# Kernel tuning notes

Measured on AMD Instinct MI355X. Metric: run time of the kernel, lower is better.

Reference implementation:

```python
import jax, jax.numpy as jnp
import numpy as np

UNITS = 512
M = 8
INPUT_DIM = 512
BATCH = 2048


def setup_inputs() -> dict:
    key = jax.random.key(0)
    ks = jax.random.split(key, 9)
    D, U = INPUT_DIM, UNITS
    fused_dim = D + U
    def glorot(k, shape):
        lim = np.sqrt(6.0 / (shape[0] + shape[1])).astype(np.float32)
        return jax.random.uniform(k, shape, jnp.float32, -lim, lim)
    return {
        "inputs": jax.random.normal(ks[0], (BATCH, D), jnp.float32),
        "elapsed": jax.random.uniform(ks[1], (BATCH, 1), jnp.float32),
        "state": jax.random.normal(ks[2], (BATCH, U * M), jnp.float32),
        "W_r": glorot(ks[3], (fused_dim, U * M)),
        "b_r": jnp.zeros((U * M,), jnp.float32),
        "W_d": glorot(ks[4], (fused_dim, U)),
        "b_d": jnp.zeros((U,), jnp.float32),
        "W_u": glorot(ks[5], (fused_dim, U * M)),
        "b_u": jnp.zeros((U * M,), jnp.float32),
    }


def reference(inputs, elapsed, state, W_r, b_r, W_d, b_d, W_u, b_u):
    B = inputs.shape[0]
    # tau_i = 10**(i/2)  =>  ln_tau_i = i * 0.5 * ln(10)
    ln_tau_table = 0.5 * jnp.log(jnp.float32(10.0)) * jnp.arange(M, dtype=jnp.float32)  # [M]
    tau_table = jnp.exp(ln_tau_table)  # [M]

    h_hat = state.reshape(B, UNITS, M)            # [B, U, M]
    h = h_hat.sum(axis=2)                          # [B, U]
    fused = jnp.concatenate([inputs, h], axis=-1)  # [B, D+U]

    # retrieval gate: softmax over M buckets of -(ln_tau_r - table)^2
    ln_tau_r = (fused @ W_r + b_r).reshape(B, UNITS, M)
    rki = jax.nn.softmax(-jnp.square(ln_tau_r - ln_tau_table), axis=2)
    q_input = jnp.sum(rki * h_hat, axis=2)         # [B, U]

    # detect (candidate) with tanh
    reset_value = jnp.concatenate([inputs, q_input], axis=1)
    qk = jnp.tanh(reset_value @ W_d + b_d)[:, :, None]  # [B, U, 1]

    # update gate
    ln_tau_s = (fused @ W_u + b_u).reshape(B, UNITS, M)
    ski = jax.nn.softmax(-jnp.square(ln_tau_s - ln_tau_table), axis=2)

    # exponential decay per bucket: elapsed [B,1] / tau [M] -> [B, M]
    exp_term = jnp.exp(-elapsed / tau_table)[:, None, :]  # [B, 1, M]
    h_hat_next = ((1.0 - ski) * h_hat + ski * qk) * exp_term  # [B, U, M]

    h_next = h_hat_next.sum(axis=2)                # [B, U]
    return h_next, h_hat_next.reshape(B, UNITS * M)
```

## Files before the change

kernel.cpp:

```cpp
#include <hip/hip_runtime.h>
#include <hip/hip_fp16.h>
#include <cmath>

#define B_SZ 2048
#define D_IN 512
#define U_N  512
#define FD   1024
#define NRU  4096
#define NRU2 8192

typedef _Float16 f16x8 __attribute__((ext_vector_type(8)));
typedef float    f32x4 __attribute__((ext_vector_type(4)));

typedef const __attribute__((address_space(1))) void glb_cv;
typedef __attribute__((address_space(3))) void lds_v;

#define TAB_INIT {0.0f, 1.15129254649702f, 2.30258509299405f, \
                  3.45387763949107f, 4.60517018598809f, 5.75646273248511f, \
                  6.90775527898214f, 8.05904782547916f}

__global__ __launch_bounds__(256) void prep_kernel(
    const float* __restrict__ inputs, const float* __restrict__ state,
    __half* __restrict__ fused, __half* __restrict__ reset)
{
    const int b = blockIdx.x;
    const int t = threadIdx.x;

    const float2 iv = *(const float2*)(inputs + (size_t)b * D_IN + t * 2);
    __half2 hv;
    hv.x = __float2half(iv.x);
    hv.y = __float2half(iv.y);
    *(__half2*)(fused + (size_t)b * FD + t * 2) = hv;
    *(__half2*)(reset + (size_t)b * FD + t * 2) = hv;

    const float4* sp = (const float4*)(state + (size_t)b * NRU + t * 16);
    float4 x0 = sp[0], x1 = sp[1], x2 = sp[2], x3 = sp[3];
    float s0 = (x0.x + x0.y) + (x0.z + x0.w) + (x1.x + x1.y) + (x1.z + x1.w);
    float s1 = (x2.x + x2.y) + (x2.z + x2.w) + (x3.x + x3.y) + (x3.z + x3.w);
    __half2 h2;
    h2.x = __float2half(s0);
    h2.y = __float2half(s1);
    *(__half2*)(fused + (size_t)b * FD + D_IN + t * 2) = h2;
}

__global__ __launch_bounds__(256) void convT3_kernel(
    const float* __restrict__ W_r, const float* __restrict__ W_u,
    const float* __restrict__ W_d, __half* __restrict__ WruT,
    __half* __restrict__ WdT)
{
    __shared__ float tile[32][33];
    const int bx = blockIdx.x;
    const float* W;
    __half* Wt;
    int N, nt;
    if (bx < 128)      { W = W_r; Wt = WruT;                        N = NRU; nt = bx * 32; }
    else if (bx < 256) { W = W_u; Wt = WruT + (size_t)NRU * FD;     N = NRU; nt = (bx - 128) * 32; }
    else               { W = W_d; Wt = WdT;                         N = U_N; nt = (bx - 256) * 32; }

    const int kt = blockIdx.y * 32;
    const int t  = threadIdx.x;
    const int c  = t & 31;
    const int r4 = t >> 5;

#pragma unroll
    for (int i = 0; i < 4; i++) {
        int r = r4 + i * 8;
        tile[r][c] = W[(size_t)(kt + r) * N + nt + c];
    }
    __syncthreads();
#pragma unroll
    for (int i = 0; i < 4; i++) {
        int rr = r4 + i * 8;
        Wt[(size_t)(nt + rr) * FD + kt + c] = __float2half(tile[c][rr]);
    }
}

template <int BM, int ACT, int EPI>
__global__ __launch_bounds__(256) void gemm_k(
    const __half* __restrict__ A, const __half* __restrict__ Bt,
    const float* __restrict__ biasA, const float* __restrict__ biasB, int nsplit,
    float* __restrict__ C, int Ncols,
    const float* __restrict__ state, __half* __restrict__ resetw,
    __half* __restrict__ skibuf, int K)
{
    extern __shared__ __align__(16) char smem[];
    __half* sA = (__half*)smem;
    __half* sB = (__half*)(smem + BM * 64);

    const int t    = threadIdx.x;
    const int m0   = blockIdx.y * BM;
    const int n0   = blockIdx.x << 7;
    const int lane = t & 63;
    const int w    = t >> 6;
    const int m16  = lane & 15;
    const int quad = lane >> 4;
    constexpr int MI = BM / 32;
    constexpr int IA = BM / 64;
    const int wm = (w & 1) * (BM / 2);
    const int wn = (w >> 1) << 6;

    f32x4 acc[MI][4];
#pragma unroll
    for (int i = 0; i < MI; i++)
#pragma unroll
        for (int j = 0; j < 4; j++)
#pragma unroll
            for (int r = 0; r < 4; r++) acc[i][j][r] = 0.f;

    const __half* gAp[IA];
    const __half* lAp[IA];
#pragma unroll
    for (int i = 0; i < IA; i++) {
        const int off = w * (BM * 16) + i * 1024 + lane * 16;
        const int row = off >> 6;
        const int kc  = (off & 63) >> 1;
        gAp[i] = A + (size_t)(m0 + row) * K + kc;
        lAp[i] = sA + ((w * (BM * 16) + i * 1024) >> 1);
    }
    const __half* gBp[2];
    const __half* lBp[2];
#pragma unroll
    for (int i = 0; i < 2; i++) {
        const int off = w * 2048 + i * 1024 + lane * 16;
        const int row = off >> 6;
        const int kc  = (off & 63) >> 1;
        gBp[i] = Bt + (size_t)(n0 + row) * K + kc;
        lBp[i] = sB + ((w * 2048 + i * 1024) >> 1);
    }

    for (int kt = 0; kt < K; kt += 32) {
        __syncthreads();
#pragma unroll
        for (int i = 0; i < IA; i++)
            __builtin_amdgcn_global_load_lds((glb_cv*)(gAp[i] + kt), (lds_v*)lAp[i], 16, 0, 0);
#pragma unroll
        for (int i = 0; i < 2; i++)
            __builtin_amdgcn_global_load_lds((glb_cv*)(gBp[i] + kt), (lds_v*)lBp[i], 16, 0, 0);
        __syncthreads();

        f16x8 af[MI], bf[4];
#pragma unroll
        for (int mi = 0; mi < MI; mi++)
            af[mi] = *(const f16x8*)(sA + (wm + mi * 16 + m16) * 32 + quad * 8);
#pragma unroll
        for (int ni = 0; ni < 4; ni++)
            bf[ni] = *(const f16x8*)(sB + (wn + ni * 16 + m16) * 32 + quad * 8);
#pragma unroll
        for (int mi = 0; mi < MI; mi++)
#pragma unroll
            for (int ni = 0; ni < 4; ni++)
                acc[mi][ni] = __builtin_amdgcn_mfma_f32_16x16x32_f16(
                    af[mi], bf[ni], acc[mi][ni], 0, 0, 0);
    }

    if constexpr (EPI == 0) {
        const float* bp  = (n0 < nsplit) ? biasA : biasB;
        const int    cb0 = (n0 < nsplit) ? n0 : n0 - nsplit;
#pragma unroll
        for (int mi = 0; mi < MI; mi++) {
#pragma unroll
            for (int ni = 0; ni < 4; ni++) {
                const int ctile = wn + ni * 16 + m16;
                const float bv = bp[cb0 + ctile];
                const int col = n0 + ctile;
#pragma unroll
                for (int r = 0; r < 4; r++) {
                    const int row = m0 + wm + mi * 16 + quad * 4 + r;
                    float v = acc[mi][ni][r] + bv;
                    if (ACT == 1) v = tanhf(v);
                    C[(size_t)row * Ncols + col] = v;
                }
            }
        }
    } else {
        __syncthreads();
        float* ebuf = (float*)smem + w * (64 * 17);
        const bool is_r = (n0 < nsplit);
        const float* bp = is_r ? biasA : biasB;
        const int cb = (is_r ? n0 : n0 - nsplit) + wn;
        const float TAB[8] = TAB_INIT;

        for (int ni = 0; ni < 4; ni++) {
            const float bv = bp[cb + ni * 16 + m16];
#pragma unroll
            for (int mi = 0; mi < 4; mi++)
#pragma unroll
                for (int r = 0; r < 4; r++)
                    ebuf[(mi * 16 + quad * 4 + r) * 17 + m16] = acc[mi][ni][r] + bv;
            __syncthreads();

            const int b = m0 + wm + lane;
#pragma unroll
            for (int j = 0; j < 2; j++) {
                const float* rowp = ebuf + lane * 17 + j * 8;
                float s[8], e[8];
                float mx = -1e30f;
#pragma unroll
                for (int i = 0; i < 8; i++) {
                    float d = rowp[i] - TAB[i];
                    s[i] = -d * d;
                    mx = fmaxf(mx, s[i]);
                }
                float sum = 0.f;
#pragma unroll
                for (int i = 0; i < 8; i++) {
                    e[i] = __expf(s[i] - mx);
                    sum += e[i];
                }
                const int c0 = cb + ni * 16 + j * 8;
                if (is_r) {
                    const float4* hh = (const float4*)(state + (size_t)b * NRU + c0);
                    float4 h0 = hh[0], h1 = hh[1];
                    float hv[8] = {h0.x, h0.y, h0.z, h0.w, h1.x, h1.y, h1.z, h1.w};
                    float qn = 0.f;
#pragma unroll
                    for (int i = 0; i < 8; i++) qn += e[i] * hv[i];
                    const float q = qn / sum;
                    resetw[(size_t)b * FD + D_IN + (c0 >> 3)] = __float2half(q);
                } else {
                    const float inv = 1.0f / sum;
                    __half2 o[4];
#pragma unroll
                    for (int i = 0; i < 4; i++) {
                        o[i].x = __float2half(e[2 * i] * inv);
                        o[i].y = __float2half(e[2 * i + 1] * inv);
                    }
                    *(uint4*)(skibuf + (size_t)b * NRU + c0) = *(uint4*)o;
                }
            }
            __syncthreads();
        }
    }
}

__global__ __launch_bounds__(256) void final_kernel(
    const __half* __restrict__ skibuf, const float* __restrict__ state,
    const float* __restrict__ qk, const float* __restrict__ elapsed,
    float* __restrict__ out0, float* __restrict__ out1)
{
    const int idx = blockIdx.x * 256 + threadIdx.x;
    const int b = idx >> 9;
    const int u = idx & 511;

    const float INV_TAU[8] = {1.0f, 0.316227766016838f, 0.1f, 0.0316227766016838f,
                              0.01f, 0.00316227766016838f, 0.001f, 0.000316227766016838f};

    const uint4 sr = *(const uint4*)(skibuf + (size_t)b * NRU + u * 8);
    const __half2* sh = (const __half2*)&sr;
    float sk[8];
#pragma unroll
    for (int i = 0; i < 4; i++) {
        sk[2 * i]     = __half2float(sh[i].x);
        sk[2 * i + 1] = __half2float(sh[i].y);
    }

    const float4* hh = (const float4*)(state + ((size_t)b * NRU + u * 8));
    float4 h0 = hh[0], h1 = hh[1];
    float h[8] = {h0.x, h0.y, h0.z, h0.w, h1.x, h1.y, h1.z, h1.w};

    const float q  = qk[(size_t)b * U_N + u];
    const float el = elapsed[b];

    float hn[8];
    float acc = 0.f;
#pragma unroll
    for (int i = 0; i < 8; i++) {
        const float et = __expf(-el * INV_TAU[i]);
        hn[i] = ((1.0f - sk[i]) * h[i] + sk[i] * q) * et;
        acc += hn[i];
    }

    float4* o = (float4*)(out1 + ((size_t)b * NRU + u * 8));
    o[0] = make_float4(hn[0], hn[1], hn[2], hn[3]);
    o[1] = make_float4(hn[4], hn[5], hn[6], hn[7]);
    out0[(size_t)b * U_N + u] = acc;
}

extern "C" void kernel_launch(void* const* d_in, const int* in_sizes, int n_in,
                              void* d_out, int out_size, void* d_ws, size_t ws_size,
                              hipStream_t stream)
{
    (void)in_sizes; (void)n_in; (void)out_size; (void)ws_size;

    const float* inputs  = (const float*)d_in[0];
    const float* elapsed = (const float*)d_in[1];
    const float* state   = (const float*)d_in[2];
    const float* W_r     = (const float*)d_in[3];
    const float* b_r     = (const float*)d_in[4];
    const float* W_d     = (const float*)d_in[5];
    const float* b_d     = (const float*)d_in[6];
    const float* W_u     = (const float*)d_in[7];
    const float* b_u     = (const float*)d_in[8];
    float* out = (float*)d_out;

    char* ws = (char*)d_ws;
    __half* fused  = (__half*)(ws);
    __half* reset  = (__half*)(ws + ((size_t)4  << 20));
    __half* WruT   = (__half*)(ws + ((size_t)8  << 20));
    __half* WdT    = (__half*)(ws + ((size_t)24 << 20));
    __half* skibuf = (__half*)(ws + ((size_t)25 << 20));
    float*  qk     = (float*) (ws + ((size_t)41 << 20));

    prep_kernel<<<B_SZ, 256, 0, stream>>>(inputs, state, fused, reset);
    convT3_kernel<<<dim3(272, FD / 32), 256, 0, stream>>>(W_r, W_u, W_d, WruT, WdT);

    gemm_k<128, 0, 1><<<dim3(NRU2 / 128, B_SZ / 128), 256, 17408, stream>>>(
        fused, WruT, b_r, b_u, NRU, nullptr, 0, state, reset, skibuf, FD);

    gemm_k<64, 1, 0><<<dim3(U_N / 128, B_SZ / 64), 256, 12288, stream>>>(
        reset, WdT, b_d, b_d, 1 << 30, qk, U_N, nullptr, nullptr, nullptr, FD);

    final_kernel<<<(B_SZ * U_N) / 256, 256, 0, stream>>>(skibuf, state, qk, elapsed, out,
                                                         out + (size_t)B_SZ * U_N);
}
```

Baseline: 231.2 us.

## Fuse final state update into detect GEMM epilogue and coalesce softmax epilogue

Result: faster. 225.8 us (-2.3%).

```diff
diff --git a/kernel.cpp b/kernel.cpp
--- a/kernel.cpp
+++ b/kernel.cpp
@@ -53,9 +53,9 @@
     const float* W;
     __half* Wt;
     int N, nt;
-    if (bx < 128)      { W = W_r; Wt = WruT;                        N = NRU; nt = bx * 32; }
-    else if (bx < 256) { W = W_u; Wt = WruT + (size_t)NRU * FD;     N = NRU; nt = (bx - 128) * 32; }
-    else               { W = W_d; Wt = WdT;                         N = U_N; nt = (bx - 256) * 32; }
+    if (bx < 128)      { W = W_r; Wt = WruT;                    N = NRU; nt = bx * 32; }
+    else if (bx < 256) { W = W_u; Wt = WruT + (size_t)NRU * FD; N = NRU; nt = (bx - 128) * 32; }
+    else               { W = W_d; Wt = WdT;                     N = U_N; nt = (bx - 256) * 32; }
 
     const int kt = blockIdx.y * 32;
     const int t  = threadIdx.x;
@@ -75,13 +75,13 @@
     }
 }
 
-template <int BM, int ACT, int EPI>
+template <int BM, int EPI>
 __global__ __launch_bounds__(256) void gemm_k(
     const __half* __restrict__ A, const __half* __restrict__ Bt,
     const float* __restrict__ biasA, const float* __restrict__ biasB, int nsplit,
-    float* __restrict__ C, int Ncols,
     const float* __restrict__ state, __half* __restrict__ resetw,
-    __half* __restrict__ skibuf, int K)
+    __half* __restrict__ skibuf, const float* __restrict__ elapsed,
+    float* __restrict__ out0, float* __restrict__ out1, int K)
 {
     extern __shared__ __align__(16) char smem[];
     __half* sA = (__half*)smem;
@@ -98,6 +98,7 @@
     constexpr int IA = BM / 64;
     const int wm = (w & 1) * (BM / 2);
     const int wn = (w >> 1) << 6;
+    const int strip = w >> 1;
 
     f32x4 acc[MI][4];
 #pragma unroll
@@ -153,70 +154,61 @@
                     af[mi], bf[ni], acc[mi][ni], 0, 0, 0);
     }
 
-    if constexpr (EPI == 0) {
-        const float* bp  = (n0 < nsplit) ? biasA : biasB;
-        const int    cb0 = (n0 < nsplit) ? n0 : n0 - nsplit;
-#pragma unroll
-        for (int mi = 0; mi < MI; mi++) {
-#pragma unroll
-            for (int ni = 0; ni < 4; ni++) {
-                const int ctile = wn + ni * 16 + m16;
-                const float bv = bp[cb0 + ctile];
-                const int col = n0 + ctile;
-#pragma unroll
-                for (int r = 0; r < 4; r++) {
-                    const int row = m0 + wm + mi * 16 + quad * 4 + r;
-                    float v = acc[mi][ni][r] + bv;
-                    if (ACT == 1) v = tanhf(v);
-                    C[(size_t)row * Ncols + col] = v;
-                }
-            }
-        }
-    } else {
+    if constexpr (EPI == 1) {
         __syncthreads();
-        float* ebuf = (float*)smem + w * (64 * 17);
+        float*  ebuf = (float*)smem;
+        __half* qbuf = (__half*)(smem + 128 * 36 * 4);
         const bool is_r = (n0 < nsplit);
         const float* bp = is_r ? biasA : biasB;
-        const int cb = (is_r ? n0 : n0 - nsplit) + wn;
+        const int n0r = is_r ? n0 : n0 - nsplit;
         const float TAB[8] = TAB_INIT;
+        const int ug  = t & 3;
+        const int s   = ug >> 1;
+        const int g   = ug & 1;
+        const int bl0 = t >> 2;
 
         for (int ni = 0; ni < 4; ni++) {
-            const float bv = bp[cb + ni * 16 + m16];
+            const float bv = bp[n0r + strip * 64 + ni * 16 + m16];
 #pragma unroll
             for (int mi = 0; mi < 4; mi++)
 #pragma unroll
                 for (int r = 0; r < 4; r++)
-                    ebuf[(mi * 16 + quad * 4 + r) * 17 + m16] = acc[mi][ni][r] + bv;
+                    ebuf[(wm + mi * 16 + quad * 4 + r) * 36 + strip * 16 + m16] =
+                        acc[mi][ni][r] + bv;
             __syncthreads();
 
-            const int b = m0 + wm + lane;
-#pragma unroll
-            for (int j = 0; j < 2; j++) {
-                const float* rowp = ebuf + lane * 17 + j * 8;
-                float s[8], e[8];
+#pragma unroll
+            for (int p = 0; p < 2; p++) {
+                const int b_loc = bl0 + p * 64;
+                const int b = m0 + b_loc;
+                const float* rowp = ebuf + b_loc * 36 + ug * 8;
+                float v[8];
+                *(float4*)&v[0] = *(const float4*)rowp;
+                *(float4*)&v[4] = *(const float4*)(rowp + 4);
+
+                float sc[8], e[8];
                 float mx = -1e30f;
 #pragma unroll
                 for (int i = 0; i < 8; i++) {
-                    float d = rowp[i] - TAB[i];
-                    s[i] = -d * d;
-                    mx = fmaxf(mx, s[i]);
+                    float d = v[i] - TAB[i];
+                    sc[i] = -d * d;
+                    mx = fmaxf(mx, sc[i]);
                 }
                 float sum = 0.f;
 #pragma unroll
                 for (int i = 0; i < 8; i++) {
-                    e[i] = __expf(s[i] - mx);
+                    e[i] = __expf(sc[i] - mx);
                     sum += e[i];
                 }
-                const int c0 = cb + ni * 16 + j * 8;
+                const int col = n0r + s * 64 + ni * 16 + g * 8;
                 if (is_r) {
-                    const float4* hh = (const float4*)(state + (size_t)b * NRU + c0);
-                    float4 h0 = hh[0], h1 = hh[1];
-                    float hv[8] = {h0.x, h0.y, h0.z, h0.w, h1.x, h1.y, h1.z, h1.w};
+                    const float4 h0 = *(const float4*)(state + (size_t)b * NRU + col);
+                    const float4 h1 = *(const float4*)(state + (size_t)b * NRU + col + 4);
+                    const float hv[8] = {h0.x, h0.y, h0.z, h0.w, h1.x, h1.y, h1.z, h1.w};
                     float qn = 0.f;
 #pragma unroll
                     for (int i = 0; i < 8; i++) qn += e[i] * hv[i];
-                    const float q = qn / sum;
-                    resetw[(size_t)b * FD + D_IN + (c0 >> 3)] = __float2half(q);
+                    qbuf[b_loc * 16 + (s * 8 + ni * 2 + g)] = __float2half(qn / sum);
                 } else {
                     const float inv = 1.0f / sum;
                     __half2 o[4];
@@ -225,55 +217,76 @@
                         o[i].x = __float2half(e[2 * i] * inv);
                         o[i].y = __float2half(e[2 * i + 1] * inv);
                     }
-                    *(uint4*)(skibuf + (size_t)b * NRU + c0) = *(uint4*)o;
+                    *(uint4*)(skibuf + (size_t)b * NRU + col) = *(uint4*)o;
                 }
             }
             __syncthreads();
         }
-    }
-}
-
-__global__ __launch_bounds__(256) void final_kernel(
-    const __half* __restrict__ skibuf, const float* __restrict__ state,
-    const float* __restrict__ qk, const float* __restrict__ elapsed,
-    float* __restrict__ out0, float* __restrict__ out1)
-{
-    const int idx = blockIdx.x * 256 + threadIdx.x;
-    const int b = idx >> 9;
-    const int u = idx & 511;
-
-    const float INV_TAU[8] = {1.0f, 0.316227766016838f, 0.1f, 0.0316227766016838f,
-                              0.01f, 0.00316227766016838f, 0.001f, 0.000316227766016838f};
-
-    const uint4 sr = *(const uint4*)(skibuf + (size_t)b * NRU + u * 8);
-    const __half2* sh = (const __half2*)&sr;
-    float sk[8];
-#pragma unroll
-    for (int i = 0; i < 4; i++) {
-        sk[2 * i]     = __half2float(sh[i].x);
-        sk[2 * i + 1] = __half2float(sh[i].y);
-    }
-
-    const float4* hh = (const float4*)(state + ((size_t)b * NRU + u * 8));
-    float4 h0 = hh[0], h1 = hh[1];
-    float h[8] = {h0.x, h0.y, h0.z, h0.w, h1.x, h1.y, h1.z, h1.w};
-
-    const float q  = qk[(size_t)b * U_N + u];
-    const float el = elapsed[b];
-
-    float hn[8];
-    float acc = 0.f;
-#pragma unroll
-    for (int i = 0; i < 8; i++) {
-        const float et = __expf(-el * INV_TAU[i]);
-        hn[i] = ((1.0f - sk[i]) * h[i] + sk[i] * q) * et;
-        acc += hn[i];
-    }
-
-    float4* o = (float4*)(out1 + ((size_t)b * NRU + u * 8));
-    o[0] = make_float4(hn[0], hn[1], hn[2], hn[3]);
-    o[1] = make_float4(hn[4], hn[5], hn[6], hn[7]);
-    out0[(size_t)b * U_N + u] = acc;
+        if (is_r) {
+            const int b_loc = t >> 1;
+            const int j = t & 1;
+            uint4 qv = *(uint4*)(qbuf + b_loc * 16 + j * 8);
+            *(uint4*)(resetw + (size_t)(m0 + b_loc) * FD + D_IN + (n0r >> 3) + j * 8) = qv;
+        }
+    } else {
+        __syncthreads();
+        float* ebuf  = (float*)smem;
+        float* etbuf = (float*)(smem + 9216);
+        const float INV_TAU[8] = {1.0f, 0.316227766016838f, 0.1f, 0.0316227766016838f,
+                                  0.01f, 0.00316227766016838f, 0.001f, 0.000316227766016838f};
+#pragma unroll
+        for (int q2 = 0; q2 < 2; q2++) {
+            const int id = t + q2 * 256;
+            const int bl = id >> 3, i = id & 7;
+            etbuf[bl * 8 + i] = __expf(-elapsed[m0 + bl] * INV_TAU[i]);
+        }
+        const int ul  = t & 31;
+        const int bl0 = t >> 5;
+
+        for (int ni = 0; ni < 4; ni++) {
+            const float bv = biasA[n0 + strip * 64 + ni * 16 + m16];
+#pragma unroll
+            for (int mi = 0; mi < MI; mi++)
+#pragma unroll
+                for (int r = 0; r < 4; r++)
+                    ebuf[(wm + mi * 16 + quad * 4 + r) * 36 + strip * 16 + m16] =
+                        tanhf(acc[mi][ni][r] + bv);
+            __syncthreads();
+
+#pragma unroll
+            for (int p = 0; p < 8; p++) {
+                const int b_loc = bl0 + p * 8;
+                const int b = m0 + b_loc;
+                const float qv = ebuf[b_loc * 36 + ul];
+                const int u = n0 + (ul >> 4) * 64 + ni * 16 + (ul & 15);
+
+                const uint4 sr = *(const uint4*)(skibuf + (size_t)b * NRU + u * 8);
+                const float4 h0 = *(const float4*)(state + (size_t)b * NRU + u * 8);
+                const float4 h1 = *(const float4*)(state + (size_t)b * NRU + u * 8 + 4);
+                const float h[8] = {h0.x, h0.y, h0.z, h0.w, h1.x, h1.y, h1.z, h1.w};
+                const __half2* sh = (const __half2*)&sr;
+                float sk[8];
+#pragma unroll
+                for (int i = 0; i < 4; i++) {
+                    float2 f2 = __half22float2(sh[i]);
+                    sk[2 * i] = f2.x;
+                    sk[2 * i + 1] = f2.y;
+                }
+                float hn[8];
+                float accs = 0.f;
+#pragma unroll
+                for (int i = 0; i < 8; i++) {
+                    const float et = etbuf[b_loc * 8 + i];
+                    hn[i] = ((1.0f - sk[i]) * h[i] + sk[i] * qv) * et;
+                    accs += hn[i];
+                }
+                *(float4*)(out1 + (size_t)b * NRU + u * 8)     = make_float4(hn[0], hn[1], hn[2], hn[3]);
+                *(float4*)(out1 + (size_t)b * NRU + u * 8 + 4) = make_float4(hn[4], hn[5], hn[6], hn[7]);
+                out0[(size_t)b * U_N + u] = accs;
+            }
+            __syncthreads();
+        }
+    }
 }
 
 extern "C" void kernel_launch(void* const* d_in, const int* in_sizes, int n_in,
@@ -299,17 +312,14 @@
     __half* WruT   = (__half*)(ws + ((size_t)8  << 20));
     __half* WdT    = (__half*)(ws + ((size_t)24 << 20));
     __half* skibuf = (__half*)(ws + ((size_t)25 << 20));
-    float*  qk     = (float*) (ws + ((size_t)41 << 20));
 
     prep_kernel<<<B_SZ, 256, 0, stream>>>(inputs, state, fused, reset);
     convT3_kernel<<<dim3(272, FD / 32), 256, 0, stream>>>(W_r, W_u, W_d, WruT, WdT);
 
-    gemm_k<128, 0, 1><<<dim3(NRU2 / 128, B_SZ / 128), 256, 17408, stream>>>(
-        fused, WruT, b_r, b_u, NRU, nullptr, 0, state, reset, skibuf, FD);
-
-    gemm_k<64, 1, 0><<<dim3(U_N / 128, B_SZ / 64), 256, 12288, stream>>>(
-        reset, WdT, b_d, b_d, 1 << 30, qk, U_N, nullptr, nullptr, nullptr, FD);
-
-    final_kernel<<<(B_SZ * U_N) / 256, 256, 0, stream>>>(skibuf, state, qk, elapsed, out,
-                                                         out + (size_t)B_SZ * U_N);
+    gemm_k<128, 1><<<dim3(NRU2 / 128, B_SZ / 128), 256, 22528, stream>>>(
+        fused, WruT, b_r, b_u, NRU, state, reset, skibuf, nullptr, nullptr, nullptr, FD);
+
+    gemm_k<64, 2><<<dim3(U_N / 128, B_SZ / 64), 256, 12288, stream>>>(
+        reset, WdT, b_d, nullptr, 1 << 30, state, nullptr, skibuf, elapsed,
+        out, out + (size_t)B_SZ * U_N, FD);
 }
```

## Double GEMM K-tile to 64 and restructure softmax epilogue with staged q writes

Applied to the files above, without the earlier changes.

Result: faster. 222.1 us (-4.0%).

```diff
diff --git a/kernel.cpp b/kernel.cpp
--- a/kernel.cpp
+++ b/kernel.cpp
@@ -53,9 +53,9 @@
     const float* W;
     __half* Wt;
     int N, nt;
-    if (bx < 128)      { W = W_r; Wt = WruT;                        N = NRU; nt = bx * 32; }
-    else if (bx < 256) { W = W_u; Wt = WruT + (size_t)NRU * FD;     N = NRU; nt = (bx - 128) * 32; }
-    else               { W = W_d; Wt = WdT;                         N = U_N; nt = (bx - 256) * 32; }
+    if (bx < 128)      { W = W_r; Wt = WruT;                    N = NRU; nt = bx * 32; }
+    else if (bx < 256) { W = W_u; Wt = WruT + (size_t)NRU * FD; N = NRU; nt = (bx - 128) * 32; }
+    else               { W = W_d; Wt = WdT;                     N = U_N; nt = (bx - 256) * 32; }
 
     const int kt = blockIdx.y * 32;
     const int t  = threadIdx.x;
@@ -75,7 +75,7 @@
     }
 }
 
-template <int BM, int ACT, int EPI>
+template <int BM, int EPI>
 __global__ __launch_bounds__(256) void gemm_k(
     const __half* __restrict__ A, const __half* __restrict__ Bt,
     const float* __restrict__ biasA, const float* __restrict__ biasB, int nsplit,
@@ -85,7 +85,7 @@
 {
     extern __shared__ __align__(16) char smem[];
     __half* sA = (__half*)smem;
-    __half* sB = (__half*)(smem + BM * 64);
+    __half* sB = (__half*)(smem + BM * 128);
 
     const int t    = threadIdx.x;
     const int m0   = blockIdx.y * BM;
@@ -95,9 +95,10 @@
     const int m16  = lane & 15;
     const int quad = lane >> 4;
     constexpr int MI = BM / 32;
-    constexpr int IA = BM / 64;
+    constexpr int IA = BM / 32;
     const int wm = (w & 1) * (BM / 2);
     const int wn = (w >> 1) << 6;
+    const int strip = w >> 1;
 
     f32x4 acc[MI][4];
 #pragma unroll
@@ -111,112 +112,114 @@
     const __half* lAp[IA];
 #pragma unroll
     for (int i = 0; i < IA; i++) {
-        const int off = w * (BM * 16) + i * 1024 + lane * 16;
-        const int row = off >> 6;
-        const int kc  = (off & 63) >> 1;
+        const int off = w * (BM * 32) + i * 1024 + lane * 16;
+        const int row = off >> 7;
+        const int kc  = (off & 127) >> 1;
         gAp[i] = A + (size_t)(m0 + row) * K + kc;
-        lAp[i] = sA + ((w * (BM * 16) + i * 1024) >> 1);
-    }
-    const __half* gBp[2];
-    const __half* lBp[2];
-#pragma unroll
-    for (int i = 0; i < 2; i++) {
-        const int off = w * 2048 + i * 1024 + lane * 16;
-        const int row = off >> 6;
-        const int kc  = (off & 63) >> 1;
+        lAp[i] = sA + ((w * (BM * 32) + i * 1024) >> 1);
+    }
+    const __half* gBp[4];
+    const __half* lBp[4];
+#pragma unroll
+    for (int i = 0; i < 4; i++) {
+        const int off = w * 4096 + i * 1024 + lane * 16;
+        const int row = off >> 7;
+        const int kc  = (off & 127) >> 1;
         gBp[i] = Bt + (size_t)(n0 + row) * K + kc;
-        lBp[i] = sB + ((w * 2048 + i * 1024) >> 1);
-    }
-
-    for (int kt = 0; kt < K; kt += 32) {
+        lBp[i] = sB + ((w * 4096 + i * 1024) >> 1);
+    }
+
+    for (int kt = 0; kt < K; kt += 64) {
         __syncthreads();
 #pragma unroll
         for (int i = 0; i < IA; i++)
             __builtin_amdgcn_global_load_lds((glb_cv*)(gAp[i] + kt), (lds_v*)lAp[i], 16, 0, 0);
 #pragma unroll
-        for (int i = 0; i < 2; i++)
+        for (int i = 0; i < 4; i++)
             __builtin_amdgcn_global_load_lds((glb_cv*)(gBp[i] + kt), (lds_v*)lBp[i], 16, 0, 0);
         __syncthreads();
 
-        f16x8 af[MI], bf[4];
-#pragma unroll
-        for (int mi = 0; mi < MI; mi++)
-            af[mi] = *(const f16x8*)(sA + (wm + mi * 16 + m16) * 32 + quad * 8);
-#pragma unroll
-        for (int ni = 0; ni < 4; ni++)
-            bf[ni] = *(const f16x8*)(sB + (wn + ni * 16 + m16) * 32 + quad * 8);
-#pragma unroll
-        for (int mi = 0; mi < MI; mi++)
+#pragma unroll
+        for (int s = 0; s < 2; s++) {
+            f16x8 af[MI], bf[4];
+#pragma unroll
+            for (int mi = 0; mi < MI; mi++)
+                af[mi] = *(const f16x8*)(sA + (wm + mi * 16 + m16) * 64 + s * 32 + quad * 8);
 #pragma unroll
             for (int ni = 0; ni < 4; ni++)
-                acc[mi][ni] = __builtin_amdgcn_mfma_f32_16x16x32_f16(
-                    af[mi], bf[ni], acc[mi][ni], 0, 0, 0);
+                bf[ni] = *(const f16x8*)(sB + (wn + ni * 16 + m16) * 64 + s * 32 + quad * 8);
+#pragma unroll
+            for (int mi = 0; mi < MI; mi++)
+#pragma unroll
+                for (int ni = 0; ni < 4; ni++)
+                    acc[mi][ni] = __builtin_amdgcn_mfma_f32_16x16x32_f16(
+                        af[mi], bf[ni], acc[mi][ni], 0, 0, 0);
+        }
     }
 
     if constexpr (EPI == 0) {
-        const float* bp  = (n0 < nsplit) ? biasA : biasB;
-        const int    cb0 = (n0 < nsplit) ? n0 : n0 - nsplit;
 #pragma unroll
         for (int mi = 0; mi < MI; mi++) {
 #pragma unroll
             for (int ni = 0; ni < 4; ni++) {
-                const int ctile = wn + ni * 16 + m16;
-                const float bv = bp[cb0 + ctile];
-                const int col = n0 + ctile;
+                const int col = n0 + wn + ni * 16 + m16;
+                const float bv = biasA[col];
 #pragma unroll
                 for (int r = 0; r < 4; r++) {
                     const int row = m0 + wm + mi * 16 + quad * 4 + r;
-                    float v = acc[mi][ni][r] + bv;
-                    if (ACT == 1) v = tanhf(v);
-                    C[(size_t)row * Ncols + col] = v;
+                    C[(size_t)row * Ncols + col] = tanhf(acc[mi][ni][r] + bv);
                 }
             }
         }
     } else {
         __syncthreads();
-        float* ebuf = (float*)smem + w * (64 * 17);
+        float*  ebuf = (float*)smem;
+        __half* qbuf = (__half*)(smem + 128 * 36 * 4);
         const bool is_r = (n0 < nsplit);
         const float* bp = is_r ? biasA : biasB;
-        const int cb = (is_r ? n0 : n0 - nsplit) + wn;
+        const int n0r = is_r ? n0 : n0 - nsplit;
         const float TAB[8] = TAB_INIT;
+        const int ug  = t & 3;
+        const int s   = ug >> 1;
+        const int g   = ug & 1;
+        const int bl0 = t >> 2;
 
         for (int ni = 0; ni < 4; ni++) {
-            const float bv = bp[cb + ni * 16 + m16];
+            const float bv = bp[n0r + strip * 64 + ni * 16 + m16];
 #pragma unroll
             for (int mi = 0; mi < 4; mi++)
 #pragma unroll
                 for (int r = 0; r < 4; r++)
-                    ebuf[(mi * 16 + quad * 4 + r) * 17 + m16] = acc[mi][ni][r] + bv;
+                    ebuf[(wm + mi * 16 + quad * 4 + r) * 36 + strip * 16 + m16] =
+                        acc[mi][ni][r] + bv;
             __syncthreads();
 
-            const int b = m0 + wm + lane;
-#pragma unroll
-            for (int j = 0; j < 2; j++) {
-                const float* rowp = ebuf + lane * 17 + j * 8;
-                float s[8], e[8];
-                float mx = -1e30f;
+#pragma unroll
+            for (int p = 0; p < 2; p++) {
+                const int b_loc = bl0 + p * 64;
+                const int b = m0 + b_loc;
+                const float* rowp = ebuf + b_loc * 36 + ug * 8;
+                float v[8];
+                *(float4*)&v[0] = *(const float4*)rowp;
+                *(float4*)&v[4] = *(const float4*)(rowp + 4);
+
+                float e[8];
+                float sum = 0.f;
 #pragma unroll
                 for (int i = 0; i < 8; i++) {
-                    float d = rowp[i] - TAB[i];
-                    s[i] = -d * d;
-                    mx = fmaxf(mx, s[i]);
-                }
-                float sum = 0.f;
-#pragma unroll
-                for (int i = 0; i < 8; i++) {
-                    e[i] = __expf(s[i] - mx);
+                    float d = v[i] - TAB[i];
+                    e[i] = __expf(-d * d);
                     sum += e[i];
                 }
-                const int c0 = cb + ni * 16 + j * 8;
+                const int col = n0r + s * 64 + ni * 16 + g * 8;
                 if (is_r) {
-                    const float4* hh = (const float4*)(state + (size_t)b * NRU + c0);
-                    float4 h0 = hh[0], h1 = hh[1];
-                    float hv[8] = {h0.x, h0.y, h0.z, h0.w, h1.x, h1.y, h1.z, h1.w};
+                    const float4 h0 = *(const float4*)(state + (size_t)b * NRU + col);
+                    const float4 h1 = *(const float4*)(state + (size_t)b * NRU + col + 4);
+                    const float hv[8] = {h0.x, h0.y, h0.z, h0.w, h1.x, h1.y, h1.z, h1.w};
                     float qn = 0.f;
 #pragma unroll
                     for (int i = 0; i < 8; i++) qn += e[i] * hv[i];
-                    const float q = qn / sum;
-                    resetw[(size_t)b * FD + D_IN + (c0 >> 3)] = __float2half(q);
+                    qbuf[b_loc * 16 + (s * 8 + ni * 2 + g)] = __float2half(qn / sum);
                 } else {
                     const float inv = 1.0f / sum;
                     __half2 o[4];
@@ -225,11 +228,17 @@
                         o[i].x = __float2half(e[2 * i] * inv);
                         o[i].y = __float2half(e[2 * i + 1] * inv);
                     }
-                    *(uint4*)(skibuf + (size_t)b * NRU + c0) = *(uint4*)o;
+                    *(uint4*)(skibuf + (size_t)b * NRU + col) = *(uint4*)o;
                 }
             }
             __syncthreads();
         }
+        if (is_r) {
+            const int b_loc = t >> 1;
+            const int j = t & 1;
+            uint4 qv = *(uint4*)(qbuf + b_loc * 16 + j * 8);
+            *(uint4*)(resetw + (size_t)(m0 + b_loc) * FD + D_IN + (n0r >> 3) + j * 8) = qv;
+        }
     }
 }
 
@@ -250,8 +259,9 @@
     float sk[8];
 #pragma unroll
     for (int i = 0; i < 4; i++) {
-        sk[2 * i]     = __half2float(sh[i].x);
-        sk[2 * i + 1] = __half2float(sh[i].y);
+        float2 f2 = __half22float2(sh[i]);
+        sk[2 * i]     = f2.x;
+        sk[2 * i + 1] = f2.y;
     }
 
     const float4* hh = (const float4*)(state + ((size_t)b * NRU + u * 8));
@@ -304,11 +314,11 @@
     prep_kernel<<<B_SZ, 256, 0, stream>>>(inputs, state, fused, reset);
     convT3_kernel<<<dim3(272, FD / 32), 256, 0, stream>>>(W_r, W_u, W_d, WruT, WdT);
 
-    gemm_k<128, 0, 1><<<dim3(NRU2 / 128, B_SZ / 128), 256, 17408, stream>>>(
+    gemm_k<128, 1><<<dim3(NRU2 / 128, B_SZ / 128), 256, 32768, stream>>>(
         fused, WruT, b_r, b_u, NRU, nullptr, 0, state, reset, skibuf, FD);
 
-    gemm_k<64, 1, 0><<<dim3(U_N / 128, B_SZ / 64), 256, 12288, stream>>>(
-        reset, WdT, b_d, b_d, 1 << 30, qk, U_N, nullptr, nullptr, nullptr, FD);
+    gemm_k<64, 0><<<dim3(U_N / 128, B_SZ / 64), 256, 24576, stream>>>(
+        reset, WdT, b_d, nullptr, 1 << 30, qk, U_N, nullptr, nullptr, nullptr, FD);
 
     final_kernel<<<(B_SZ * U_N) / 256, 256, 0, stream>>>(skibuf, state, qk, elapsed, out,
                                                          out + (size_t)B_SZ * U_N);
```
